# Kernel optimization log

Hardware: AMD Instinct MI355X
Metric: run time of the kernel (lower is better)

Reference implementation:

```python
import jax, jax.numpy as jnp
import numpy as np

# --- module constants (from init_kwargs) ---
BETA = 0.95
UTE = 1.0001
DELAY = 7
CHOSEN_W1 = 0.5
THRESHOLD = 1.0      # snntorch Leaky default threshold
ALPHA = 2.0          # snntorch ATan surrogate default alpha
T, B = 4096, 4096
SPIKE_PROB = 0.02    # sparse binary spike trains


@jax.custom_vjp
def spike_fn(x):
    # Heaviside forward; ATan surrogate gradient in backward (snntorch default)
    return (x > 0).astype(x.dtype)

def _spike_fwd(x):
    return spike_fn(x), x

def _spike_bwd(x, g):
    return (g * (ALPHA / 2.0) / (1.0 + (jnp.pi / 2.0 * ALPHA * x) ** 2),)

spike_fn.defvjp(_spike_fwd, _spike_bwd)


def setup_inputs() -> dict:
    key = jax.random.key(0)
    k1, _ = jax.random.split(key)
    spike_seq = (jax.random.uniform(k1, (T, B, 2)) < SPIKE_PROB).astype(jnp.float32)
    # calculate_weights(delay): w1 = chosen_w1; w2 = ute - beta**delay * w1
    w1 = CHOSEN_W1
    w2 = UTE - BETA ** DELAY * w1
    W = jnp.array([[w1, w2]], dtype=jnp.float32)  # fc.weight, shape [1, 2]
    return {"spike_seq": spike_seq, "W": W}


def reference(spike_seq, W):
    # spike_seq: [T, B, 2], W: [1, 2] -> spk_rec: [T, B, 1]
    # Precompute all linear currents in one GEMM (same math as per-step fc)
    cur_seq = jnp.einsum('tbi,oi->tbo', spike_seq, W)  # [T, B, 1]

    def step(mem, cur):
        # snntorch Leaky (reset_mechanism='subtract'):
        #   reset computed from PREVIOUS mem (detached heaviside)
        reset = (mem > THRESHOLD).astype(mem.dtype)
        mem_new = BETA * mem + cur - reset * THRESHOLD
        spk = spike_fn(mem_new - THRESHOLD)
        return mem_new, spk

    mem0 = jnp.zeros((spike_seq.shape[1], 1), dtype=spike_seq.dtype)
    _, spk_rec = jax.lax.scan(step, mem0, cur_seq)
    return spk_rec
```

## Files before the change

### kernel.cpp

```cpp
#include <hip/hip_runtime.h>
#include <stdint.h>


#define T_STEPS 4096
#define B_NEUR  4096
#define NCHUNK  16
#define CH_W    16
#define WARM_W  48
#define KG      (T_STEPS / 16)

typedef float f4v __attribute__((ext_vector_type(4)));

__global__ __launch_bounds__(256) void fmfm_compress(
    const f4v*  __restrict__ sp4,
    uint32_t*   __restrict__ codes)
{
    const int tid = blockIdx.x * 256 + threadIdx.x;
    const int b2  = tid & (B_NEUR / 2 - 1);
    const int kg  = tid >> 11;
    const f4v* p = sp4 + (size_t)kg * 16 * (B_NEUR / 2) + b2;
    uint32_t we = 0, wo = 0;
    #pragma unroll
    for (int i = 0; i < 16; ++i) {
        f4v s = __builtin_nontemporal_load(p + (size_t)i * (B_NEUR / 2));
        uint32_t ce = (s.x != 0.0f ? 1u : 0u) | (s.y != 0.0f ? 2u : 0u);
        uint32_t co = (s.z != 0.0f ? 1u : 0u) | (s.w != 0.0f ? 2u : 0u);
        we |= ce << (2 * i);
        wo |= co << (2 * i);
    }
    *reinterpret_cast<uint2*>(codes + (size_t)kg * B_NEUR + 2 * b2) =
        make_uint2(we, wo);
}

__global__ __launch_bounds__(256) void fmfm_scanA(
    const uint32_t* __restrict__ codes,
    const float*    __restrict__ W,
    float*          __restrict__ out,
    uint4*          __restrict__ spec)
{
    __shared__ float2   lut2[16];
    __shared__ uint32_t lbits[256];

    const float w1  = W[0];
    const float w2  = W[1];
    const float w12 = __fadd_rn(w1, w2);

    if (threadIdx.x < 16) {
        uint32_t e = threadIdx.x;
        uint32_t c0 = e & 3u, c1 = (e >> 2) & 3u;
        float2 v;
        v.x = (c0 & 1u) ? ((c0 & 2u) ? w12 : w1) : ((c0 & 2u) ? w2 : 0.0f);
        v.y = (c1 & 1u) ? ((c1 & 2u) ? w12 : w1) : ((c1 & 2u) ? w2 : 0.0f);
        lut2[e] = v;
    }
    __syncthreads();

    const int tid = blockIdx.x * 256 + threadIdx.x;
    const int b   = tid & (B_NEUR - 1);
    const int c   = tid >> 12;
    const int b0  = (blockIdx.x * 256) & (B_NEUR - 1);
    const int body_w0 = c * CH_W;
    const int w_start = (body_w0 >= WARM_W) ? body_w0 - WARM_W : 0;
    const int w_end   = body_w0 + CH_W;
    const uint32_t* cp = codes + b;

#define CLD(IDX) cp[(size_t)((IDX) < w_end ? (IDX) : (w_end - 1)) * B_NEUR]
#define DECODE2(WORD, D)                                                  \
    {                                                                     \
        _Pragma("unroll")                                                 \
        for (int _j = 0; _j < 8; ++_j)                                    \
            D[_j] = lut2[((WORD) >> (4 * _j)) & 0xFu];                    \
    }
#define STEPN(CUR)                                                        \
    {                                                                     \
        float _m = __fsub_rn(__fadd_rn(__fmul_rn(0.95f, mem), (CUR)),     \
                             rst);                                        \
        rst = (_m > 1.0f) ? 1.0f : 0.0f;                                  \
        mem = _m;                                                         \
    }
#define STEPB(CUR, POS)                                                   \
    {                                                                     \
        float _m = __fsub_rn(__fadd_rn(__fmul_rn(0.95f, mem), (CUR)),     \
                             rst);                                        \
        uint32_t _sb = (_m > 1.0f) ? 1u : 0u;                             \
        bits |= _sb << (POS);                                             \
        rst = _sb ? 1.0f : 0.0f;                                          \
        mem = _m;                                                         \
    }
#define CHAIN16N(D)                                                       \
    {                                                                     \
        _Pragma("unroll")                                                 \
        for (int _j = 0; _j < 8; ++_j) { STEPN(D[_j].x) STEPN(D[_j].y) }  \
    }
#define CHAIN16B(D, HALF)                                                 \
    {                                                                     \
        _Pragma("unroll")                                                 \
        for (int _j = 0; _j < 8; ++_j) {                                  \
            STEPB(D[_j].x, ((HALF) << 4) + 2 * _j)                        \
            STEPB(D[_j].y, ((HALF) << 4) + 2 * _j + 1)                    \
        }                                                                 \
    }

    uint32_t pa = CLD(w_start);
    uint32_t pb = CLD(w_start + 1);
    uint32_t pc = CLD(w_start + 2);
    uint32_t pd = CLD(w_start + 3);

    float2 dA[8], dB[8];
    DECODE2(pa, dA)

    float mem = 0.0f, rst = 0.0f;

    for (int iw = w_start; iw < body_w0; iw += 2) {
        uint32_t t0 = CLD(iw + 4);
        DECODE2(pb, dB)
        CHAIN16N(dA)
        pa = pb; pb = pc; pc = pd; pd = t0;
        uint32_t t1 = CLD(iw + 5);
        DECODE2(pb, dA)
        CHAIN16N(dB)
        pa = pb; pb = pc; pc = pd; pd = t1;
    }

    const float sm = mem;
    const float sr = rst;

    const int q  = threadIdx.x & 63;
    const int th = threadIdx.x >> 6;
    for (int iw = body_w0; iw < w_end; iw += 2) {
        uint32_t bits = 0;
        uint32_t t0 = CLD(iw + 4);
        DECODE2(pb, dB)
        CHAIN16B(dA, 0)
        pa = pb; pb = pc; pc = pd; pd = t0;
        uint32_t t1 = CLD(iw + 5);
        DECODE2(pb, dA)
        CHAIN16B(dB, 1)
        pa = pb; pb = pc; pc = pd; pd = t1;

        lbits[threadIdx.x] = bits;
        __syncthreads();
        const uint4 bw = *reinterpret_cast<const uint4*>(&lbits[4 * q]);
        float* qp = out + (size_t)iw * 16 * B_NEUR + b0 + 4 * q;
        #pragma unroll
        for (int r = 0; r < 8; ++r) {
            const int tp = th * 8 + r;
            f4v v;
            v.x = ((bw.x >> tp) & 1u) ? 1.0f : 0.0f;
            v.y = ((bw.y >> tp) & 1u) ? 1.0f : 0.0f;
            v.z = ((bw.z >> tp) & 1u) ? 1.0f : 0.0f;
            v.w = ((bw.w >> tp) & 1u) ? 1.0f : 0.0f;
            *reinterpret_cast<f4v*>(qp + (size_t)tp * B_NEUR) = v;
        }
        __syncthreads();
    }

    uint4 sv;
    sv.x = __float_as_uint(sm);
    sv.y = (sr != 0.0f) ? 1u : 0u;
    sv.z = __float_as_uint(mem);
    sv.w = (rst != 0.0f) ? 1u : 0u;
    spec[(size_t)c * B_NEUR + b] = sv;

#undef CLD
#undef DECODE2
#undef STEPN
#undef STEPB
#undef CHAIN16N
#undef CHAIN16B
}

__global__ __launch_bounds__(64) void fmfm_scanB(
    const uint32_t* __restrict__ codes,
    const float*    __restrict__ W,
    float*          __restrict__ out,
    const uint4*    __restrict__ spec)
{
    const int b = blockIdx.x * 64 + threadIdx.x;
    const float w1  = W[0];
    const float w2  = W[1];
    const float w12 = __fadd_rn(w1, w2);

    float mem = 0.0f, rst = 0.0f;
    uint4 sn = spec[b];
    for (int c = 0; c < NCHUNK; ++c) {
        uint4 s = sn;
        if (c + 1 < NCHUNK) sn = spec[(size_t)(c + 1) * B_NEUR + b];
        bool ok = (s.x == __float_as_uint(mem)) &&
                  ((s.y != 0u) == (rst != 0.0f));
        if (ok) {
            mem = __uint_as_float(s.z);
            rst = s.w ? 1.0f : 0.0f;
        } else {
            for (int wi = 0; wi < CH_W; ++wi) {
                uint32_t w = codes[(size_t)(c * CH_W + wi) * B_NEUR + b];
                float* q = out + (size_t)(c * CH_W + wi) * 16 * B_NEUR + b;
                #pragma unroll
                for (int j = 0; j < 16; ++j) {
                    uint32_t cc = (w >> (2 * j)) & 3u;
                    float cur = (cc & 1u) ? ((cc & 2u) ? w12 : w1)
                                          : ((cc & 2u) ? w2 : 0.0f);
                    float m = __fsub_rn(__fadd_rn(__fmul_rn(0.95f, mem), cur),
                                        rst);
                    rst = (m > 1.0f) ? 1.0f : 0.0f;
                    mem = m;
                    q[(size_t)j * B_NEUR] = rst;
                }
            }
        }
    }
}

__global__ __launch_bounds__(64) void fmfm_scan_fused(
    const float2* __restrict__ sp, const float* __restrict__ W,
    float* __restrict__ out)
{
    const int b = blockIdx.x * 64 + threadIdx.x;
    const float w1 = W[0];
    const float w2 = W[1];
    const float2* p = sp + b;
    float* q = out + b;
    float mem = 0.0f, rst = 0.0f;
    #pragma unroll 8
    for (int t = 0; t < T_STEPS; ++t) {
        float2 s = p[(size_t)t * B_NEUR];
        float cur = __fadd_rn(__fmul_rn(s.x, w1), __fmul_rn(s.y, w2));
        float m = __fsub_rn(__fadd_rn(__fmul_rn(0.95f, mem), cur), rst);
        float spk = (m > 1.0f) ? 1.0f : 0.0f;
        q[(size_t)t * B_NEUR] = spk;
        mem = m;
        rst = spk;
    }
}

extern "C" void kernel_launch(void* const* d_in, const int* in_sizes, int n_in,
                              void* d_out, int out_size, void* d_ws, size_t ws_size,
                              hipStream_t stream) {
    const f4v*   sp4 = (const f4v*)d_in[0];
    const float* W   = (const float*)d_in[1];
    float*       out = (float*)d_out;

    const size_t codes_bytes = (size_t)KG * B_NEUR * 4;
    const size_t spec_bytes  = (size_t)NCHUNK * B_NEUR * 16;
    if (ws_size < codes_bytes + spec_bytes) {
        fmfm_scan_fused<<<dim3(B_NEUR / 64), dim3(64), 0, stream>>>(
            (const float2*)d_in[0], W, out);
        return;
    }
    uint32_t* codes = (uint32_t*)d_ws;
    uint4*    spec  = (uint4*)((char*)d_ws + codes_bytes);

    fmfm_compress<<<dim3(KG * (B_NEUR / 2) / 256), dim3(256), 0, stream>>>(sp4, codes);
    fmfm_scanA<<<dim3(NCHUNK * B_NEUR / 256), dim3(256), 0, stream>>>(codes, W, out, spec);
    fmfm_scanB<<<dim3(B_NEUR / 64), dim3(64), 0, stream>>>(codes, W, out, spec);
}
```

Baseline: 58.04 us.

## Write packed spike bits from scans and expand to floats in separate kernel

The scan kernels now store 32-bit packed spike words to a workspace instead of writing float outputs directly. The LDS transpose and the two barriers per chunk are removed, and a new fully parallel expand kernel turns the bits into the float output. The code-word prefetch is also widened from 4 to 8 words per group. This aims to take the 64 MB float write off the latency-bound scan and give it to a bandwidth-friendly kernel, at the cost of one extra launch and a small bit buffer round-trip.

```diff
diff --git a/kernel.cpp b/kernel.cpp
--- a/kernel.cpp
+++ b/kernel.cpp
@@ -8,6 +8,7 @@
 #define CH_W    16
 #define WARM_W  48
 #define KG      (T_STEPS / 16)
+#define NWORDS  (T_STEPS / 32)
 
 typedef float f4v __attribute__((ext_vector_type(4)));
 
@@ -35,11 +36,10 @@
 __global__ __launch_bounds__(256) void fmfm_scanA(
     const uint32_t* __restrict__ codes,
     const float*    __restrict__ W,
-    float*          __restrict__ out,
+    uint32_t*       __restrict__ bits_out,
     uint4*          __restrict__ spec)
 {
-    __shared__ float2   lut2[16];
-    __shared__ uint32_t lbits[256];
+    __shared__ float2 lut2[16];
 
     const float w1  = W[0];
     const float w2  = W[1];
@@ -58,7 +58,6 @@
     const int tid = blockIdx.x * 256 + threadIdx.x;
     const int b   = tid & (B_NEUR - 1);
     const int c   = tid >> 12;
-    const int b0  = (blockIdx.x * 256) & (B_NEUR - 1);
     const int body_w0 = c * CH_W;
     const int w_start = (body_w0 >= WARM_W) ? body_w0 - WARM_W : 0;
     const int w_end   = body_w0 + CH_W;
@@ -100,59 +99,54 @@
             STEPB(D[_j].y, ((HALF) << 4) + 2 * _j + 1)                    \
         }                                                                 \
     }
-
-    uint32_t pa = CLD(w_start);
-    uint32_t pb = CLD(w_start + 1);
-    uint32_t pc = CLD(w_start + 2);
-    uint32_t pd = CLD(w_start + 3);
+#define PF8(G)                                                            \
+    t0 = CLD((G) + 8);  t1 = CLD((G) + 9);  t2 = CLD((G) + 10);           \
+    t3 = CLD((G) + 11); t4 = CLD((G) + 12); t5 = CLD((G) + 13);           \
+    t6 = CLD((G) + 14); t7 = CLD((G) + 15);
+#define ROT8()                                                            \
+    c0 = t0; c1 = t1; c2 = t2; c3 = t3;                                   \
+    c4 = t4; c5 = t5; c6 = t6; c7 = t7;
+#define STB(IDX) bits_out[(size_t)(IDX) * B_NEUR + b] = bits;
+
+    uint32_t c0 = CLD(w_start);     uint32_t c1 = CLD(w_start + 1);
+    uint32_t c2 = CLD(w_start + 2); uint32_t c3 = CLD(w_start + 3);
+    uint32_t c4 = CLD(w_start + 4); uint32_t c5 = CLD(w_start + 5);
+    uint32_t c6 = CLD(w_start + 6); uint32_t c7 = CLD(w_start + 7);
+    uint32_t t0, t1, t2, t3, t4, t5, t6, t7;
 
     float2 dA[8], dB[8];
-    DECODE2(pa, dA)
+    DECODE2(c0, dA)
 
     float mem = 0.0f, rst = 0.0f;
 
-    for (int iw = w_start; iw < body_w0; iw += 2) {
-        uint32_t t0 = CLD(iw + 4);
-        DECODE2(pb, dB)
-        CHAIN16N(dA)
-        pa = pb; pb = pc; pc = pd; pd = t0;
-        uint32_t t1 = CLD(iw + 5);
-        DECODE2(pb, dA)
-        CHAIN16N(dB)
-        pa = pb; pb = pc; pc = pd; pd = t1;
+    for (int g = w_start; g < body_w0; g += 8) {
+        PF8(g)
+        DECODE2(c1, dB) CHAIN16N(dA)
+        DECODE2(c2, dA) CHAIN16N(dB)
+        DECODE2(c3, dB) CHAIN16N(dA)
+        DECODE2(c4, dA) CHAIN16N(dB)
+        DECODE2(c5, dB) CHAIN16N(dA)
+        DECODE2(c6, dA) CHAIN16N(dB)
+        DECODE2(c7, dB) CHAIN16N(dA)
+        DECODE2(t0, dA) CHAIN16N(dB)
+        ROT8()
     }
 
     const float sm = mem;
     const float sr = rst;
 
-    const int q  = threadIdx.x & 63;
-    const int th = threadIdx.x >> 6;
-    for (int iw = body_w0; iw < w_end; iw += 2) {
+    for (int g = body_w0; g < w_end; g += 8) {
+        PF8(g)
         uint32_t bits = 0;
-        uint32_t t0 = CLD(iw + 4);
-        DECODE2(pb, dB)
-        CHAIN16B(dA, 0)
-        pa = pb; pb = pc; pc = pd; pd = t0;
-        uint32_t t1 = CLD(iw + 5);
-        DECODE2(pb, dA)
-        CHAIN16B(dB, 1)
-        pa = pb; pb = pc; pc = pd; pd = t1;
-
-        lbits[threadIdx.x] = bits;
-        __syncthreads();
-        const uint4 bw = *reinterpret_cast<const uint4*>(&lbits[4 * q]);
-        float* qp = out + (size_t)iw * 16 * B_NEUR + b0 + 4 * q;
-        #pragma unroll
-        for (int r = 0; r < 8; ++r) {
-            const int tp = th * 8 + r;
-            f4v v;
-            v.x = ((bw.x >> tp) & 1u) ? 1.0f : 0.0f;
-            v.y = ((bw.y >> tp) & 1u) ? 1.0f : 0.0f;
-            v.z = ((bw.z >> tp) & 1u) ? 1.0f : 0.0f;
-            v.w = ((bw.w >> tp) & 1u) ? 1.0f : 0.0f;
-            *reinterpret_cast<f4v*>(qp + (size_t)tp * B_NEUR) = v;
-        }
-        __syncthreads();
+        DECODE2(c1, dB) CHAIN16B(dA, 0)
+        DECODE2(c2, dA) CHAIN16B(dB, 1) STB((g + 1) >> 1) bits = 0;
+        DECODE2(c3, dB) CHAIN16B(dA, 0)
+        DECODE2(c4, dA) CHAIN16B(dB, 1) STB((g + 3) >> 1) bits = 0;
+        DECODE2(c5, dB) CHAIN16B(dA, 0)
+        DECODE2(c6, dA) CHAIN16B(dB, 1) STB((g + 5) >> 1) bits = 0;
+        DECODE2(c7, dB) CHAIN16B(dA, 0)
+        DECODE2(t0, dA) CHAIN16B(dB, 1) STB((g + 7) >> 1)
+        ROT8()
     }
 
     uint4 sv;
@@ -168,12 +162,15 @@
 #undef STEPB
 #undef CHAIN16N
 #undef CHAIN16B
+#undef PF8
+#undef ROT8
+#undef STB
 }
 
 __global__ __launch_bounds__(64) void fmfm_scanB(
     const uint32_t* __restrict__ codes,
     const float*    __restrict__ W,
-    float*          __restrict__ out,
+    uint32_t*       __restrict__ bits_out,
     const uint4*    __restrict__ spec)
 {
     const int b = blockIdx.x * 64 + threadIdx.x;
@@ -192,9 +189,9 @@
             mem = __uint_as_float(s.z);
             rst = s.w ? 1.0f : 0.0f;
         } else {
+            uint32_t bits = 0;
             for (int wi = 0; wi < CH_W; ++wi) {
                 uint32_t w = codes[(size_t)(c * CH_W + wi) * B_NEUR + b];
-                float* q = out + (size_t)(c * CH_W + wi) * 16 * B_NEUR + b;
                 #pragma unroll
                 for (int j = 0; j < 16; ++j) {
                     uint32_t cc = (w >> (2 * j)) & 3u;
@@ -202,12 +199,40 @@
                                           : ((cc & 2u) ? w2 : 0.0f);
                     float m = __fsub_rn(__fadd_rn(__fmul_rn(0.95f, mem), cur),
                                         rst);
-                    rst = (m > 1.0f) ? 1.0f : 0.0f;
+                    uint32_t sb = (m > 1.0f) ? 1u : 0u;
+                    bits |= sb << (((wi & 1) << 4) + j);
+                    rst = sb ? 1.0f : 0.0f;
                     mem = m;
-                    q[(size_t)j * B_NEUR] = rst;
+                }
+                if (wi & 1) {
+                    bits_out[(size_t)((c * CH_W + wi) >> 1) * B_NEUR + b] = bits;
+                    bits = 0;
                 }
             }
         }
+    }
+}
+
+__global__ __launch_bounds__(256) void fmfm_expand(
+    const uint32_t* __restrict__ bits,
+    float*          __restrict__ out)
+{
+    const int tid = blockIdx.x * 256 + threadIdx.x;
+    const int b4  = tid & 1023;
+    const int w   = (tid >> 10) & 127;
+    const int q   = tid >> 17;
+    const uint4 bw = *reinterpret_cast<const uint4*>(
+        bits + (size_t)w * B_NEUR + (size_t)b4 * 4);
+    float* qp = out + ((size_t)w * 32 + q * 8) * B_NEUR + (size_t)b4 * 4;
+    #pragma unroll
+    for (int r = 0; r < 8; ++r) {
+        const int tp = q * 8 + r;
+        f4v v;
+        v.x = ((bw.x >> tp) & 1u) ? 1.0f : 0.0f;
+        v.y = ((bw.y >> tp) & 1u) ? 1.0f : 0.0f;
+        v.z = ((bw.z >> tp) & 1u) ? 1.0f : 0.0f;
+        v.w = ((bw.w >> tp) & 1u) ? 1.0f : 0.0f;
+        *reinterpret_cast<f4v*>(qp + (size_t)r * B_NEUR) = v;
     }
 }
 
@@ -241,16 +266,19 @@
     float*       out = (float*)d_out;
 
     const size_t codes_bytes = (size_t)KG * B_NEUR * 4;
+    const size_t bits_bytes  = (size_t)NWORDS * B_NEUR * 4;
     const size_t spec_bytes  = (size_t)NCHUNK * B_NEUR * 16;
-    if (ws_size < codes_bytes + spec_bytes) {
+    if (ws_size < codes_bytes + bits_bytes + spec_bytes) {
         fmfm_scan_fused<<<dim3(B_NEUR / 64), dim3(64), 0, stream>>>(
             (const float2*)d_in[0], W, out);
         return;
     }
     uint32_t* codes = (uint32_t*)d_ws;
-    uint4*    spec  = (uint4*)((char*)d_ws + codes_bytes);
+    uint32_t* bits  = (uint32_t*)((char*)d_ws + codes_bytes);
+    uint4*    spec  = (uint4*)((char*)d_ws + codes_bytes + bits_bytes);
 
     fmfm_compress<<<dim3(KG * (B_NEUR / 2) / 256), dim3(256), 0, stream>>>(sp4, codes);
-    fmfm_scanA<<<dim3(NCHUNK * B_NEUR / 256), dim3(256), 0, stream>>>(codes, W, out, spec);
-    fmfm_scanB<<<dim3(B_NEUR / 64), dim3(64), 0, stream>>>(codes, W, out, spec);
-}
+    fmfm_scanA<<<dim3(NCHUNK * B_NEUR / 256), dim3(256), 0, stream>>>(codes, W, bits, spec);
+    fmfm_scanB<<<dim3(B_NEUR / 64), dim3(64), 0, stream>>>(codes, W, bits, spec);
+    fmfm_expand<<<dim3(NWORDS * (B_NEUR / 4) * 4 / 256), dim3(256), 0, stream>>>(bits, out);
+}
```

Result: slower. 61.58 us (+6.1%).
